# Kernel tuning notes

Hardware: AMD Instinct MI355X
Metric: run time of the kernel (lower is better)

## Reference

```python
import jax, jax.numpy as jnp
import numpy as np

GROUPS = 32
EPS = 1e-6  # flax.linen.GroupNorm default


def group_norm(x, scale, bias):
    B, H, W, C = x.shape
    xg = x.reshape(B, H, W, GROUPS, C // GROUPS)
    mean = jnp.mean(xg, axis=(1, 2, 4), keepdims=True)
    var = jnp.var(xg, axis=(1, 2, 4), keepdims=True)
    xn = (xg - mean) * jax.lax.rsqrt(var + EPS)
    return xn.reshape(B, H, W, C) * scale + bias


def setup_inputs() -> dict:
    key = jax.random.key(0)
    ks = jax.random.split(key, 8)
    B, H, W, C = 8, 64, 64, 128
    s = C ** -0.5  # fan-in style init scale for 1x1 conv kernels
    return {
        "x": jax.random.normal(ks[0], (B, H, W, C), dtype=jnp.float32),
        "gn_scale": jnp.ones((C,), dtype=jnp.float32),
        "gn_bias": jnp.zeros((C,), dtype=jnp.float32),
        "wq": jax.random.normal(ks[1], (C, C), dtype=jnp.float32) * s,
        "bq": jnp.zeros((C,), dtype=jnp.float32),
        "wk": jax.random.normal(ks[2], (C, C), dtype=jnp.float32) * s,
        "bk": jnp.zeros((C,), dtype=jnp.float32),
        "wv": jax.random.normal(ks[3], (C, C), dtype=jnp.float32) * s,
        "bv": jnp.zeros((C,), dtype=jnp.float32),
        "wo": jax.random.normal(ks[4], (C, C), dtype=jnp.float32) * s,
        "bo": jnp.zeros((C,), dtype=jnp.float32),
    }


def reference(x, gn_scale, gn_bias, wq, bq, wk, bk, wv, bv, wo, bo):
    B, H, W, C = x.shape
    N = H * W
    h = group_norm(x, gn_scale, gn_bias)                       # [B,H,W,C]
    hf = h.reshape(B, N, C)
    q = hf @ wq + bq                                           # 1x1 conv == per-position matmul
    k = hf @ wk + bk
    v = hf @ wv + bv
    w_ = jnp.einsum('bqd,bkd->bqk', q, k) * (C ** -0.5)        # [B,N,N] full score matrix
    w_ = jax.nn.softmax(w_, axis=2)
    o = jnp.einsum('bqk,bkd->bqd', w_, v)                      # [B,N,C]
    o = o @ wo + bo
    return x + o.reshape(B, H, W, C)
```

## Files before the change

### kernel.cpp

```cpp
#include <hip/hip_runtime.h>
#include <hip/hip_bf16.h>

#define NN 4096
#define CC 128
#define SCALE 0.088388347648318447f
#define LOG2E 1.4426950408889634f

typedef __attribute__((ext_vector_type(8))) short short8v;
typedef __attribute__((ext_vector_type(4))) float f32x4;
typedef __attribute__((ext_vector_type(16))) float f32x16;

#define Z16 {0.f,0.f,0.f,0.f,0.f,0.f,0.f,0.f,0.f,0.f,0.f,0.f,0.f,0.f,0.f,0.f}

__device__ __forceinline__ short f2bf(float f) {
  unsigned u = __float_as_uint(f);
  u = (u + 0x7FFFu + ((u >> 16) & 1u)) >> 16;
  return (short)u;
}
__device__ __forceinline__ float bf2f(short s) {
  return __uint_as_float(((unsigned)(unsigned short)s) << 16);
}
__device__ __forceinline__ unsigned pk2bf(float lo, float hi) {
  unsigned r;
  asm("v_cvt_pk_bf16_f32 %0, %1, %2" : "=v"(r) : "v"(lo), "v"(hi));
  return r;
}
__device__ __forceinline__ f32x4 mfma16(short8v a, short8v b, f32x4 c) {
  return __builtin_amdgcn_mfma_f32_16x16x32_bf16(a, b, c, 0, 0, 0);
}
__device__ __forceinline__ f32x16 mfma32(short8v a, short8v b, f32x16 c) {
  return __builtin_amdgcn_mfma_f32_32x32x16_bf16(a, b, c, 0, 0, 0);
}
__device__ __forceinline__ void gload16(const void* g, void* l) {
  __builtin_amdgcn_global_load_lds(
      (const __attribute__((address_space(1))) unsigned*)g,
      (__attribute__((address_space(3))) unsigned*)l, 16, 0, 0);
}

__global__ __launch_bounds__(256) void prep_k(
    const float* __restrict__ x,
    const float* __restrict__ wq, const float* __restrict__ wk,
    const float* __restrict__ wv, const float* __restrict__ wo,
    const float* __restrict__ bq, short* __restrict__ wT,
    float* __restrict__ bqs, float* __restrict__ mean,
    float* __restrict__ rstd) {
  if (blockIdx.x >= 256) {
    int gid = (blockIdx.x - 256) * 256 + threadIdx.x;
    int widx = gid >> 14, e = gid & 16383;
    int kk = e >> 7, n = e & 127;
    const float* src = (widx == 0) ? wq : (widx == 1) ? wk
                     : (widx == 2) ? wv : wo;
    float v = src[kk * 128 + n];
    if (widx == 0) v *= SCALE * LOG2E;
    wT[widx * 16384 + n * 128 + kk] = f2bf(v);
    if (gid < 128) bqs[gid] = bq[gid] * SCALE * LOG2E;
    return;
  }
  int bg = blockIdx.x;
  const float* xp = x + (size_t)(bg >> 5) * NN * CC + (bg & 31) * 4;
  float s = 0.f, ss = 0.f;
  for (int n = threadIdx.x; n < NN; n += 256) {
    float4 v = *reinterpret_cast<const float4*>(xp + (size_t)n * CC);
    s  += v.x + v.y + v.z + v.w;
    ss += v.x * v.x + v.y * v.y + v.z * v.z + v.w * v.w;
  }
  #pragma unroll
  for (int m = 1; m < 64; m <<= 1) {
    s += __shfl_xor(s, m, 64);
    ss += __shfl_xor(ss, m, 64);
  }
  __shared__ float rs[4], rss[4];
  int wid = threadIdx.x >> 6;
  if ((threadIdx.x & 63) == 0) { rs[wid] = s; rss[wid] = ss; }
  __syncthreads();
  if (threadIdx.x == 0) {
    s = rs[0] + rs[1] + rs[2] + rs[3];
    ss = rss[0] + rss[1] + rss[2] + rss[3];
    float mu = s * (1.f / 16384.f);
    float var = ss * (1.f / 16384.f) - mu * mu;
    mean[bg] = mu;
    rstd[bg] = rsqrtf(var + 1e-6f);
  }
}

__global__ __launch_bounds__(256) void fqkv_k(
    const float* __restrict__ x, const float* __restrict__ mean,
    const float* __restrict__ rstd, const float* __restrict__ gsc,
    const float* __restrict__ gbi, const short* __restrict__ wT,
    const float* __restrict__ bqs, const float* __restrict__ bk,
    const float* __restrict__ bv, short* __restrict__ qout,
    short* __restrict__ kout, short* __restrict__ vtout) {
  __shared__ short wlds[128][136];
  int lane = threadIdx.x & 63, wid = threadIdx.x >> 6;
  int row0 = blockIdx.x * 64 + wid * 16;
  int arow = row0 + (lane & 15);
  int q4 = lane >> 4;
  int bidx = arow >> 12;
  short8v a[4];
  #pragma unroll
  for (int dt = 0; dt < 4; ++dt) {
    int c0 = dt * 32 + q4 * 8;
    float4 v0 = *reinterpret_cast<const float4*>(x + (size_t)arow * CC + c0);
    float4 v1 = *reinterpret_cast<const float4*>(x + (size_t)arow * CC + c0 + 4);
    int g0 = bidx * 32 + (c0 >> 2);
    float mu0 = mean[g0], r0 = rstd[g0];
    float mu1 = mean[g0 + 1], r1 = rstd[g0 + 1];
    float4 s0 = *reinterpret_cast<const float4*>(gsc + c0);
    float4 s1 = *reinterpret_cast<const float4*>(gsc + c0 + 4);
    float4 b0 = *reinterpret_cast<const float4*>(gbi + c0);
    float4 b1 = *reinterpret_cast<const float4*>(gbi + c0 + 4);
    union { short s[8]; short8v v; } pk;
    pk.s[0] = f2bf((v0.x - mu0) * r0 * s0.x + b0.x);
    pk.s[1] = f2bf((v0.y - mu0) * r0 * s0.y + b0.y);
    pk.s[2] = f2bf((v0.z - mu0) * r0 * s0.z + b0.z);
    pk.s[3] = f2bf((v0.w - mu0) * r0 * s0.w + b0.w);
    pk.s[4] = f2bf((v1.x - mu1) * r1 * s1.x + b1.x);
    pk.s[5] = f2bf((v1.y - mu1) * r1 * s1.y + b1.y);
    pk.s[6] = f2bf((v1.z - mu1) * r1 * s1.z + b1.z);
    pk.s[7] = f2bf((v1.w - mu1) * r1 * s1.w + b1.w);
    a[dt] = pk.v;
  }
  for (int ph = 0; ph < 3; ++ph) {
    if (ph) __syncthreads();
    const short* w = wT + ph * 16384;
    for (int i = threadIdx.x; i < 2048; i += 256) {
      int n = i >> 4, kk = (i & 15) << 3;
      *reinterpret_cast<short8v*>(&wlds[n][kk]) =
          *reinterpret_cast<const short8v*>(w + n * 128 + kk);
    }
    __syncthreads();
    const float* bias = (ph == 0) ? bqs : (ph == 1) ? bk : bv;
    f32x4 zero = {0.f, 0.f, 0.f, 0.f};
    f32x4 acc[8];
    #pragma unroll
    for (int nt = 0; nt < 8; ++nt) acc[nt] = zero;
    #pragma unroll
    for (int nt = 0; nt < 8; ++nt) {
      #pragma unroll
      for (int kk = 0; kk < 4; ++kk) {
        short8v b = *reinterpret_cast<const short8v*>(
            &wlds[nt * 16 + (lane & 15)][kk * 32 + q4 * 8]);
        acc[nt] = mfma16(a[kk], b, acc[nt]);
      }
    }
    short* dst = (ph == 0) ? qout : (ph == 1) ? kout : vtout;
    #pragma unroll
    for (int nt = 0; nt < 8; ++nt) {
      #pragma unroll
      for (int r = 0; r < 4; ++r) {
        int row = row0 + q4 * 4 + r;
        int col = nt * 16 + (lane & 15);
        float v = acc[nt][r] + bias[col];
        if (ph == 2) {
          int b_ = row >> 12, n = row & 4095;
          dst[((size_t)b_ * 128 + col) * 4096 + n] = f2bf(v);
        } else {
          dst[(size_t)row * 128 + col] = f2bf(v);
        }
      }
    }
  }
}

template <int S>
__global__ __launch_bounds__(256, 3) void attn3_k(
    const short* __restrict__ q, const short* __restrict__ k,
    const short* __restrict__ vt, short* __restrict__ opart,
    float* __restrict__ ls) {
  constexpr int KVLEN = NN / S;
  constexpr int NIT = KVLEN / 32;
  __shared__ short8v smem_v[2048];
  char* smem = (char*)smem_v;
  const int tid = threadIdx.x;
  const int lane = tid & 63, warp = tid >> 6;
  const int hh = lane >> 5, ql = lane & 31;
  const int split = (int)blockIdx.x % S;
  const int qb_lin = (int)blockIdx.x / S;
  const int b = qb_lin >> 5, qblk = qb_lin & 31;
  const int kv0 = split * KVLEN;

  const size_t bqko = (size_t)b * NN * CC;
  short8v qf[8];
  {
    int qrow = qblk * 128 + warp * 32 + ql;
    const short* qp = q + bqko + (size_t)qrow * CC + hh * 8;
    #pragma unroll
    for (int dc = 0; dc < 8; ++dc)
      qf[dc] = *reinterpret_cast<const short8v*>(qp + dc * 16);
  }
  const char* kg = (const char*)(k + bqko);
  const char* vg = (const char*)(vt + (size_t)b * CC * NN);

  auto stage = [&](int buf, int it) {
    const int kvo = kv0 + it * 32;
    char* base = smem + buf * 16384;
    #pragma unroll
    for (int p = 0; p < 2; ++p) {
      int c = p * 256 + warp * 64 + lane;
      int krow = c >> 4, kj = c & 15;
      gload16(kg + (size_t)(kvo + krow) * 256 + 16 * (kj ^ (krow & 7)),
              base + p * 4096 + warp * 1024);
      int vd = c >> 2, vj = c & 3;
      gload16(vg + (size_t)vd * (NN * 2) + (size_t)kvo * 2 +
                  16 * (vj ^ ((vd >> 1) & 3)),
              base + 8192 + p * 4096 + warp * 1024);
    }
  };

  f32x16 oacc[4] = {Z16, Z16, Z16, Z16};
  float l_run = 0.f;

  stage(0, 0);
  asm volatile("s_waitcnt vmcnt(0)" ::: "memory");
  __builtin_amdgcn_s_barrier();

  const int swzK = (ql & 7) << 4;
  const int swzV = (ql & 6) << 3;
  for (int it = 0; it < NIT; ++it) {
    const int cur = it & 1;
    if (it + 1 < NIT) stage(cur ^ 1, it + 1);

    const char* kr_p = smem + cur * 16384 + ql * 256;
    f32x16 sT = Z16;
    #pragma unroll
    for (int dc = 0; dc < 8; ++dc) {
      short8v kf = *reinterpret_cast<const short8v*>(
          kr_p + ((32 * dc + 16 * hh) ^ swzK));
      sT = mfma32(kf, qf[dc], sT);
    }

    float rsum = 0.f;
    #pragma unroll
    for (int r = 0; r < 16; ++r) {
      float p = exp2f(sT[r]);
      sT[r] = p; rsum += p;
    }
    rsum += __shfl_xor(rsum, 32);
    l_run += rsum;

    const char* vb_ = smem + cur * 16384 + 8192;
    #pragma unroll
    for (int st = 0; st < 2; ++st) {
      const int rb = 8 * st;
      unsigned w0, w1, w2, w3;
      {
        unsigned xlo = pk2bf(sT[rb + 0], sT[rb + 1]);
        unsigned xhi = pk2bf(sT[rb + 4], sT[rb + 5]);
        unsigned xlx = (unsigned)__shfl_xor((int)xlo, 32);
        unsigned xhx = (unsigned)__shfl_xor((int)xhi, 32);
        w0 = hh ? xhx : xlo;
        w2 = hh ? xhi : xlx;
      }
      {
        unsigned xlo = pk2bf(sT[rb + 2], sT[rb + 3]);
        unsigned xhi = pk2bf(sT[rb + 6], sT[rb + 7]);
        unsigned xlx = (unsigned)__shfl_xor((int)xlo, 32);
        unsigned xhx = (unsigned)__shfl_xor((int)xhi, 32);
        w1 = hh ? xhx : xlo;
        w3 = hh ? xhi : xlx;
      }
      union { unsigned u[4]; short8v v; } pu;
      pu.u[0] = w0; pu.u[1] = w1; pu.u[2] = w2; pu.u[3] = w3;
      #pragma unroll
      for (int dt = 0; dt < 4; ++dt) {
        const char* vr_p = vb_ + (32 * dt + ql) * 64;
        short8v vf = *reinterpret_cast<const short8v*>(
            vr_p + ((32 * st + 16 * hh) ^ swzV));
        oacc[dt] = mfma32(pu.v, vf, oacc[dt]);
      }
    }

    asm volatile("s_waitcnt vmcnt(0)" ::: "memory");
    __builtin_amdgcn_s_barrier();
  }

  float rinv = 1.f / l_run;
  short* op = opart + ((size_t)(split * 8 + b) * NN + qblk * 128 + warp * 32) * CC;
  #pragma unroll
  for (int r = 0; r < 16; ++r) {
    int qp = (r & 3) + 8 * (r >> 2) + 4 * hh;
    float ri = __shfl(rinv, qp);
    #pragma unroll
    for (int dt = 0; dt < 4; ++dt)
      op[(size_t)qp * CC + 32 * dt + ql] = f2bf(oacc[dt][r] * ri);
  }
  if (hh == 0) {
    size_t ix = (size_t)(split * 8 + b) * NN + qblk * 128 + warp * 32 + ql;
    ls[ix] = l_run;
  }
}

template <int S>
__global__ __launch_bounds__(256) void projoc_k(const short* __restrict__ opart,
    const float* __restrict__ ls, const short* __restrict__ wT,
    const float* __restrict__ bias, const float* __restrict__ x,
    float* __restrict__ out) {
  __shared__ short wlds[128][136];
  int lane = threadIdx.x & 63, wid = threadIdx.x >> 6;
  for (int i = threadIdx.x; i < 2048; i += 256) {
    int n = i >> 4, kk = (i & 15) << 3;
    *reinterpret_cast<short8v*>(&wlds[n][kk]) =
        *reinterpret_cast<const short8v*>(wT + n * 128 + kk);
  }
  int row0 = blockIdx.x * 64 + wid * 16;
  int arow = row0 + (lane & 15);
  int q4 = lane >> 4;
  float wgt[S];
  {
    float tot = 0.f;
    #pragma unroll
    for (int s = 0; s < S; ++s) {
      wgt[s] = ls[(size_t)s * 32768 + arow];
      tot += wgt[s];
    }
    float inv = 1.f / tot;
    #pragma unroll
    for (int s = 0; s < S; ++s) wgt[s] *= inv;
  }
  short8v a[4];
  #pragma unroll
  for (int dt = 0; dt < 4; ++dt) {
    int c0 = dt * 32 + q4 * 8;
    float acc8[8] = {0.f, 0.f, 0.f, 0.f, 0.f, 0.f, 0.f, 0.f};
    #pragma unroll
    for (int s = 0; s < S; ++s) {
      short8v v = *reinterpret_cast<const short8v*>(
          opart + ((size_t)s * 32768 + arow) * CC + c0);
      #pragma unroll
      for (int e = 0; e < 8; ++e) acc8[e] += wgt[s] * bf2f(v[e]);
    }
    union { short s[8]; short8v v; } pk;
    #pragma unroll
    for (int e = 0; e < 8; ++e) pk.s[e] = f2bf(acc8[e]);
    a[dt] = pk.v;
  }
  __syncthreads();
  f32x4 zero = {0.f, 0.f, 0.f, 0.f};
  f32x4 acc[8];
  #pragma unroll
  for (int nt = 0; nt < 8; ++nt) acc[nt] = zero;
  #pragma unroll
  for (int nt = 0; nt < 8; ++nt) {
    #pragma unroll
    for (int kk = 0; kk < 4; ++kk) {
      short8v b = *reinterpret_cast<const short8v*>(
          &wlds[nt * 16 + (lane & 15)][kk * 32 + q4 * 8]);
      acc[nt] = mfma16(a[kk], b, acc[nt]);
    }
  }
  #pragma unroll
  for (int nt = 0; nt < 8; ++nt) {
    #pragma unroll
    for (int r = 0; r < 4; ++r) {
      int row = row0 + q4 * 4 + r;
      int col = nt * 16 + (lane & 15);
      out[(size_t)row * 128 + col] =
          acc[nt][r] + bias[col] + x[(size_t)row * 128 + col];
    }
  }
}

extern "C" void kernel_launch(void* const* d_in, const int* in_sizes, int n_in,
                              void* d_out, int out_size, void* d_ws, size_t ws_size,
                              hipStream_t stream) {
  (void)in_sizes; (void)n_in; (void)out_size;
  const float* x   = (const float*)d_in[0];
  const float* gsc = (const float*)d_in[1];
  const float* gbi = (const float*)d_in[2];
  const float* wq  = (const float*)d_in[3];
  const float* bq  = (const float*)d_in[4];
  const float* wk  = (const float*)d_in[5];
  const float* bk  = (const float*)d_in[6];
  const float* wv  = (const float*)d_in[7];
  const float* bv  = (const float*)d_in[8];
  const float* wo  = (const float*)d_in[9];
  const float* bo  = (const float*)d_in[10];
  float* out = (float*)d_out;

  char* ws = (char*)d_ws;
  constexpr size_t OFF_WT   = 0;
  constexpr size_t OFF_BQS  = 131072;
  constexpr size_t OFF_MEAN = 131584;
  constexpr size_t OFF_RSTD = 132608;
  constexpr size_t OFF_QB   = 133632;
  constexpr size_t OFF_KB   = OFF_QB + 8388608;
  constexpr size_t OFF_VT   = OFF_KB + 8388608;
  constexpr size_t OFF_OP   = OFF_VT + 8388608;
  constexpr size_t NEED4 = OFF_OP + 4 * 8388608 + 4 * 131072;
  constexpr size_t NEED2 = OFF_OP + 2 * 8388608 + 2 * 131072;

  short* wT   = (short*)(ws + OFF_WT);
  float* bqs  = (float*)(ws + OFF_BQS);
  float* mean = (float*)(ws + OFF_MEAN);
  float* rstd = (float*)(ws + OFF_RSTD);
  short* qb   = (short*)(ws + OFF_QB);
  short* kb   = (short*)(ws + OFF_KB);
  short* vtb  = (short*)(ws + OFF_VT);
  short* opart= (short*)(ws + OFF_OP);
  const int S = (ws_size >= NEED4) ? 4 : (ws_size >= NEED2) ? 2 : 1;
  float* ls = (float*)(ws + OFF_OP + (size_t)S * 8388608);

  prep_k<<<512, 256, 0, stream>>>(x, wq, wk, wv, wo, bq, wT, bqs, mean, rstd);
  fqkv_k<<<512, 256, 0, stream>>>(x, mean, rstd, gsc, gbi, wT, bqs, bk, bv,
                                  qb, kb, vtb);
  if (S == 4) {
    attn3_k<4><<<1024, 256, 0, stream>>>(qb, kb, vtb, opart, ls);
    projoc_k<4><<<512, 256, 0, stream>>>(opart, ls, wT + 49152, bo, x, out);
  } else if (S == 2) {
    attn3_k<2><<<512, 256, 0, stream>>>(qb, kb, vtb, opart, ls);
    projoc_k<2><<<512, 256, 0, stream>>>(opart, ls, wT + 49152, bo, x, out);
  } else {
    attn3_k<1><<<256, 256, 0, stream>>>(qb, kb, vtb, opart, ls);
    projoc_k<1><<<512, 256, 0, stream>>>(opart, ls, wT + 49152, bo, x, out);
  }
}
```

Baseline: 143.1 us.

## Coalesce group-norm stats with atomics and drop P-matrix lane shuffles in attention

The group-norm statistics pass now has each block read a contiguous 128-row chunk fully coalesced and atomically add per-group partial sums into zeroed accumulators, replacing the strided per-group read. fqkv derives mean and rstd from those sums. In the attention loop, the cross-half shuffles that rearranged bf16 P values are removed: the V fragment is instead loaded as two 8-byte pieces at matching offsets, and the row-sum shuffle moves out of the loop to the end. This adds a memset launch and float atomics, which make the sum order nondeterministic.

```diff
diff --git a/kernel.cpp b/kernel.cpp
--- a/kernel.cpp
+++ b/kernel.cpp
@@ -42,8 +42,8 @@
     const float* __restrict__ wq, const float* __restrict__ wk,
     const float* __restrict__ wv, const float* __restrict__ wo,
     const float* __restrict__ bq, short* __restrict__ wT,
-    float* __restrict__ bqs, float* __restrict__ mean,
-    float* __restrict__ rstd) {
+    float* __restrict__ bqs, float* __restrict__ macc,
+    float* __restrict__ vacc) {
   if (blockIdx.x >= 256) {
     int gid = (blockIdx.x - 256) * 256 + threadIdx.x;
     int widx = gid >> 14, e = gid & 16383;
@@ -56,36 +56,32 @@
     if (gid < 128) bqs[gid] = bq[gid] * SCALE * LOG2E;
     return;
   }
-  int bg = blockIdx.x;
-  const float* xp = x + (size_t)(bg >> 5) * NN * CC + (bg & 31) * 4;
+  int b = blockIdx.x >> 5, rc = blockIdx.x & 31;
+  const float4* xp = reinterpret_cast<const float4*>(
+      x + (size_t)b * NN * CC + (size_t)rc * 128 * CC);
+  int tid = threadIdx.x;
   float s = 0.f, ss = 0.f;
-  for (int n = threadIdx.x; n < NN; n += 256) {
-    float4 v = *reinterpret_cast<const float4*>(xp + (size_t)n * CC);
+  #pragma unroll
+  for (int j = 0; j < 16; ++j) {
+    float4 v = xp[tid + 256 * j];
     s  += v.x + v.y + v.z + v.w;
     ss += v.x * v.x + v.y * v.y + v.z * v.z + v.w * v.w;
   }
-  #pragma unroll
-  for (int m = 1; m < 64; m <<= 1) {
-    s += __shfl_xor(s, m, 64);
-    ss += __shfl_xor(ss, m, 64);
-  }
-  __shared__ float rs[4], rss[4];
-  int wid = threadIdx.x >> 6;
-  if ((threadIdx.x & 63) == 0) { rs[wid] = s; rss[wid] = ss; }
+  __shared__ float as_[256], ass_[256];
+  as_[tid] = s; ass_[tid] = ss;
   __syncthreads();
-  if (threadIdx.x == 0) {
-    s = rs[0] + rs[1] + rs[2] + rs[3];
-    ss = rss[0] + rss[1] + rss[2] + rss[3];
-    float mu = s * (1.f / 16384.f);
-    float var = ss * (1.f / 16384.f) - mu * mu;
-    mean[bg] = mu;
-    rstd[bg] = rsqrtf(var + 1e-6f);
+  if (tid < 32) {
+    float ts = 0.f, tss = 0.f;
+    #pragma unroll
+    for (int j = 0; j < 8; ++j) { ts += as_[tid + 32 * j]; tss += ass_[tid + 32 * j]; }
+    atomicAdd(&macc[b * 32 + tid], ts);
+    atomicAdd(&vacc[b * 32 + tid], tss);
   }
 }
 
 __global__ __launch_bounds__(256) void fqkv_k(
-    const float* __restrict__ x, const float* __restrict__ mean,
-    const float* __restrict__ rstd, const float* __restrict__ gsc,
+    const float* __restrict__ x, const float* __restrict__ macc,
+    const float* __restrict__ vacc, const float* __restrict__ gsc,
     const float* __restrict__ gbi, const short* __restrict__ wT,
     const float* __restrict__ bqs, const float* __restrict__ bk,
     const float* __restrict__ bv, short* __restrict__ qout,
@@ -103,8 +99,10 @@
     float4 v0 = *reinterpret_cast<const float4*>(x + (size_t)arow * CC + c0);
     float4 v1 = *reinterpret_cast<const float4*>(x + (size_t)arow * CC + c0 + 4);
     int g0 = bidx * 32 + (c0 >> 2);
-    float mu0 = mean[g0], r0 = rstd[g0];
-    float mu1 = mean[g0 + 1], r1 = rstd[g0 + 1];
+    float mu0 = macc[g0] * (1.f / 16384.f);
+    float r0 = rsqrtf(vacc[g0] * (1.f / 16384.f) - mu0 * mu0 + 1e-6f);
+    float mu1 = macc[g0 + 1] * (1.f / 16384.f);
+    float r1 = rsqrtf(vacc[g0 + 1] * (1.f / 16384.f) - mu1 * mu1 + 1e-6f);
     float4 s0 = *reinterpret_cast<const float4*>(gsc + c0);
     float4 s1 = *reinterpret_cast<const float4*>(gsc + c0 + 4);
     float4 b0 = *reinterpret_cast<const float4*>(gbi + c0);
@@ -163,7 +161,7 @@
 }
 
 template <int S>
-__global__ __launch_bounds__(256, 3) void attn3_k(
+__global__ __launch_bounds__(256, 3) void attn5_k(
     const short* __restrict__ q, const short* __restrict__ k,
     const short* __restrict__ vt, short* __restrict__ opart,
     float* __restrict__ ls) {
@@ -235,38 +233,24 @@
       float p = exp2f(sT[r]);
       sT[r] = p; rsum += p;
     }
-    rsum += __shfl_xor(rsum, 32);
     l_run += rsum;
 
     const char* vb_ = smem + cur * 16384 + 8192;
     #pragma unroll
     for (int st = 0; st < 2; ++st) {
-      const int rb = 8 * st;
-      unsigned w0, w1, w2, w3;
-      {
-        unsigned xlo = pk2bf(sT[rb + 0], sT[rb + 1]);
-        unsigned xhi = pk2bf(sT[rb + 4], sT[rb + 5]);
-        unsigned xlx = (unsigned)__shfl_xor((int)xlo, 32);
-        unsigned xhx = (unsigned)__shfl_xor((int)xhi, 32);
-        w0 = hh ? xhx : xlo;
-        w2 = hh ? xhi : xlx;
-      }
-      {
-        unsigned xlo = pk2bf(sT[rb + 2], sT[rb + 3]);
-        unsigned xhi = pk2bf(sT[rb + 6], sT[rb + 7]);
-        unsigned xlx = (unsigned)__shfl_xor((int)xlo, 32);
-        unsigned xhx = (unsigned)__shfl_xor((int)xhi, 32);
-        w1 = hh ? xhx : xlo;
-        w3 = hh ? xhi : xlx;
-      }
       union { unsigned u[4]; short8v v; } pu;
-      pu.u[0] = w0; pu.u[1] = w1; pu.u[2] = w2; pu.u[3] = w3;
+      #pragma unroll
+      for (int w = 0; w < 4; ++w)
+        pu.u[w] = pk2bf(sT[8 * st + 2 * w], sT[8 * st + 2 * w + 1]);
+      const int o1 = (32 * st + 8 * hh) ^ swzV;
+      const int o2 = (32 * st + 8 * hh + 16) ^ swzV;
       #pragma unroll
       for (int dt = 0; dt < 4; ++dt) {
         const char* vr_p = vb_ + (32 * dt + ql) * 64;
-        short8v vf = *reinterpret_cast<const short8v*>(
-            vr_p + ((32 * st + 16 * hh) ^ swzV));
-        oacc[dt] = mfma32(pu.v, vf, oacc[dt]);
+        union { unsigned long long d[2]; short8v v; } vf;
+        vf.d[0] = *reinterpret_cast<const unsigned long long*>(vr_p + o1);
+        vf.d[1] = *reinterpret_cast<const unsigned long long*>(vr_p + o2);
+        oacc[dt] = mfma32(pu.v, vf.v, oacc[dt]);
       }
     }
 
@@ -274,6 +258,7 @@
     __builtin_amdgcn_s_barrier();
   }
 
+  l_run += __shfl_xor(l_run, 32);
   float rinv = 1.f / l_run;
   short* op = opart + ((size_t)(split * 8 + b) * NN + qblk * 128 + warp * 32) * CC;
   #pragma unroll
@@ -380,8 +365,8 @@
   char* ws = (char*)d_ws;
   constexpr size_t OFF_WT   = 0;
   constexpr size_t OFF_BQS  = 131072;
-  constexpr size_t OFF_MEAN = 131584;
-  constexpr size_t OFF_RSTD = 132608;
+  constexpr size_t OFF_MACC = 131584;
+  constexpr size_t OFF_VACC = 132608;
   constexpr size_t OFF_QB   = 133632;
   constexpr size_t OFF_KB   = OFF_QB + 8388608;
   constexpr size_t OFF_VT   = OFF_KB + 8388608;
@@ -391,8 +376,8 @@
 
   short* wT   = (short*)(ws + OFF_WT);
   float* bqs  = (float*)(ws + OFF_BQS);
-  float* mean = (float*)(ws + OFF_MEAN);
-  float* rstd = (float*)(ws + OFF_RSTD);
+  float* macc = (float*)(ws + OFF_MACC);
+  float* vacc = (float*)(ws + OFF_VACC);
   short* qb   = (short*)(ws + OFF_QB);
   short* kb   = (short*)(ws + OFF_KB);
   short* vtb  = (short*)(ws + OFF_VT);
@@ -400,17 +385,18 @@
   const int S = (ws_size >= NEED4) ? 4 : (ws_size >= NEED2) ? 2 : 1;
   float* ls = (float*)(ws + OFF_OP + (size_t)S * 8388608);
 
-  prep_k<<<512, 256, 0, stream>>>(x, wq, wk, wv, wo, bq, wT, bqs, mean, rstd);
-  fqkv_k<<<512, 256, 0, stream>>>(x, mean, rstd, gsc, gbi, wT, bqs, bk, bv,
+  hipMemsetAsync(ws + OFF_MACC, 0, 2048, stream);
+  prep_k<<<512, 256, 0, stream>>>(x, wq, wk, wv, wo, bq, wT, bqs, macc, vacc);
+  fqkv_k<<<512, 256, 0, stream>>>(x, macc, vacc, gsc, gbi, wT, bqs, bk, bv,
                                   qb, kb, vtb);
   if (S == 4) {
-    attn3_k<4><<<1024, 256, 0, stream>>>(qb, kb, vtb, opart, ls);
+    attn5_k<4><<<1024, 256, 0, stream>>>(qb, kb, vtb, opart, ls);
     projoc_k<4><<<512, 256, 0, stream>>>(opart, ls, wT + 49152, bo, x, out);
   } else if (S == 2) {
-    attn3_k<2><<<512, 256, 0, stream>>>(qb, kb, vtb, opart, ls);
+    attn5_k<2><<<512, 256, 0, stream>>>(qb, kb, vtb, opart, ls);
     projoc_k<2><<<512, 256, 0, stream>>>(opart, ls, wT + 49152, bo, x, out);
   } else {
-    attn3_k<1><<<256, 256, 0, stream>>>(qb, kb, vtb, opart, ls);
+    attn5_k<1><<<256, 256, 0, stream>>>(qb, kb, vtb, opart, ls);
     projoc_k<1><<<512, 256, 0, stream>>>(opart, ls, wT + 49152, bo, x, out);
   }
 }
```

After: 131.7 us. -8.0%, faster.
